# Performance work log

Measured on AMD Instinct MI355X. Metric: run time of the kernel, lower is better.

The kernel has to match this reference:

```python
import jax, jax.numpy as jnp
import numpy as np

D_MODEL = 2048
SEQ_LEN = 16   # R is built for context_window=16 in the original module
BATCH = 256


def make_rotary_matrix(m, d):
    # Faithful to get_rotary_matrix: theta = 10000 ** (-2*(i-1)/d)  (note the i-1 bug kept)
    pos = np.arange(m, dtype=np.float64)[:, None]            # [m,1]
    i = np.arange(d // 2, dtype=np.float64)[None, :]         # [1,d/2]
    theta = 10000.0 ** (-2.0 * (i - 1.0) / d)
    ang = pos * theta                                         # [m, d/2]
    cos, sin = np.cos(ang), np.sin(ang)
    R = np.zeros((m, d, d), dtype=np.float32)
    idx = np.arange(d // 2)
    R[:, 2 * idx, 2 * idx] = cos
    R[:, 2 * idx, 2 * idx + 1] = -sin
    R[:, 2 * idx + 1, 2 * idx] = sin
    R[:, 2 * idx + 1, 2 * idx + 1] = cos
    return jnp.asarray(R)


def setup_inputs() -> dict:
    key = jax.random.key(0)
    kx, kq, kk, kv = jax.random.split(key, 4)
    s = 1.0 / np.sqrt(D_MODEL)
    return {
        "x": jax.random.normal(kx, (BATCH, SEQ_LEN, D_MODEL), dtype=jnp.float32),
        "w_q": jax.random.normal(kq, (D_MODEL, D_MODEL), dtype=jnp.float32) * s,
        "w_k": jax.random.normal(kk, (D_MODEL, D_MODEL), dtype=jnp.float32) * s,
        "w_v": jax.random.normal(kv, (D_MODEL, D_MODEL), dtype=jnp.float32) * s,
    }


def reference(x, w_q, w_k, w_v):
    b, m, d = x.shape
    R = make_rotary_matrix(SEQ_LEN, d)[:m]                    # [m,d,d]
    # nn.Linear(bias=False): y = x @ W^T
    q = jnp.einsum("bmd,ed->bme", x, w_q)
    k = jnp.einsum("bmd,ed->bme", x, w_k)
    v = jnp.einsum("bmd,ed->bme", x, w_v)
    # dense per-position rotary rotation via bmm: (q.transpose(0,1) @ R[:m]).transpose(0,1)
    q_rot = jnp.einsum("bmd,mde->bme", q, R)
    k_rot = jnp.einsum("bmd,mde->bme", k, R)
    # scaled_dot_product_attention (dropout treated as eval-mode / disabled)
    scores = jnp.einsum("bme,bne->bmn", q_rot, k_rot) / jnp.sqrt(jnp.float32(d))
    attn = jax.nn.softmax(scores, axis=-1)
    return jnp.einsum("bmn,bne->bme", attn, v)
```

## Files before the change

### kernel.cpp

```cpp
#include <hip/hip_runtime.h>


#define D 2048
#define SEQLEN 16
#define NBATCH 256
#define NROWS (NBATCH * SEQLEN)
#define NX (NROWS * D)
#define NW (D * D)

#define BM 128
#define BN 192
#define BK 64
#define NKT (D / BK)
#define LDSPB ((BM + BN) * BK)

typedef __attribute__((ext_vector_type(8))) short bf16x8;
typedef __attribute__((ext_vector_type(4))) float f32x4;

__device__ __forceinline__ unsigned short f32_to_bf16(float f) {
  unsigned u = __float_as_uint(f);
  unsigned r = 0x7fffu + ((u >> 16) & 1u);
  return (unsigned short)((u + r) >> 16);
}
__device__ __forceinline__ float bf16lo_to_f32(unsigned u) { return __uint_as_float(u << 16); }
__device__ __forceinline__ float bf16hi_to_f32(unsigned u) { return __uint_as_float(u & 0xffff0000u); }

__device__ __forceinline__ bool detect_f32(const ushort* __restrict__ w) {
  int crazy = 0;
#pragma unroll
  for (int i = 0; i < 64; ++i) {
    float v = __uint_as_float((unsigned)w[i] << 16);
    if (!(__builtin_fabsf(v) < 256.0f)) ++crazy;
  }
  return crazy >= 3;
}

__device__ __forceinline__ void glds16(const void* g, void* l) {
  __builtin_amdgcn_global_load_lds(
      (const __attribute__((address_space(1))) void*)g,
      (__attribute__((address_space(3))) void*)l, 16, 0, 0);
}

__global__ __launch_bounds__(256) void convert_inputs(
    const void* __restrict__ x, const void* __restrict__ wq,
    const void* __restrict__ wk, const void* __restrict__ wv,
    ushort* __restrict__ xb, ushort* __restrict__ wqb,
    ushort* __restrict__ wkb, ushort* __restrict__ wvb) {
  if (!detect_f32((const ushort*)wq)) return;
  const float* srcs[4] = {(const float*)x, (const float*)wq, (const float*)wk, (const float*)wv};
  ushort* dsts[4] = {xb, wqb, wkb, wvb};
  const int ns[4] = {NX, NW, NW, NW};
  const int stride = gridDim.x * blockDim.x;
#pragma unroll
  for (int s = 0; s < 4; ++s) {
    const float* __restrict__ src = srcs[s];
    ushort* __restrict__ dst = dsts[s];
    const int n8 = ns[s] / 8;
    for (int i = blockIdx.x * blockDim.x + threadIdx.x; i < n8; i += stride) {
      float4 a = ((const float4*)src)[i * 2];
      float4 b = ((const float4*)src)[i * 2 + 1];
      uint4 o;
      o.x = (unsigned)f32_to_bf16(a.x) | ((unsigned)f32_to_bf16(a.y) << 16);
      o.y = (unsigned)f32_to_bf16(a.z) | ((unsigned)f32_to_bf16(a.w) << 16);
      o.z = (unsigned)f32_to_bf16(b.x) | ((unsigned)f32_to_bf16(b.y) << 16);
      o.w = (unsigned)f32_to_bf16(b.z) | ((unsigned)f32_to_bf16(b.w) << 16);
      ((uint4*)dst)[i] = o;
    }
  }
}

__global__ __launch_bounds__(256, 2) void qkv_rope_gemm(
    const void* __restrict__ Xr, const void* __restrict__ Wqr,
    const void* __restrict__ Wkr, const void* __restrict__ Wvr,
    const ushort* __restrict__ xb, const ushort* __restrict__ wqb,
    const ushort* __restrict__ wkb, const ushort* __restrict__ wvb,
    ushort* __restrict__ Ov, float* __restrict__ Sp) {
  __shared__ __align__(16) ushort lds[2][LDSPB];

  const bool f32in = detect_f32((const ushort*)Wqr);
  const ushort* __restrict__ X  = f32in ? xb  : (const ushort*)Xr;
  const ushort* __restrict__ Wq = f32in ? wqb : (const ushort*)Wqr;
  const ushort* __restrict__ Wk = f32in ? wkb : (const ushort*)Wkr;
  const ushort* __restrict__ Wv = f32in ? wvb : (const ushort*)Wvr;

  const int m0 = (blockIdx.x >> 5) * BM;
  const int eb = blockIdx.x & 31;
  const int e0 = eb * 64;

  const int t = threadIdx.x;
  const int wave = t >> 6, lane = t & 63;
  const int quad = lane >> 4, l16 = lane & 15;
  const int wr = wave >> 1, wc = wave & 1;

  const int srow = t >> 3;
  const int scol = ((t & 7) ^ (srow & 7)) * 8;
  const ushort* gA = X + (size_t)(m0 + srow) * D + scol;
  const ushort* gB[6];
#pragma unroll
  for (int c = 0; c < 6; ++c) {
    const ushort* Wz = (c < 2) ? Wq : (c < 4) ? Wk : Wv;
    gB[c] = Wz + (size_t)(e0 + (c & 1) * 32 + srow) * D + scol;
  }

  f32x4 acc[4][6] = {};

  auto STAGE = [&](int b, int kt) {
    const int kc = kt * BK;
#pragma unroll
    for (int c = 0; c < 4; ++c)
      glds16(gA + (size_t)c * 32 * D + kc, &lds[b][c * 2048 + t * 8]);
#pragma unroll
    for (int c = 0; c < 6; ++c)
      glds16(gB[c] + kc, &lds[b][BM * BK + c * 2048 + t * 8]);
  };

  STAGE(0, 0);
  STAGE(1, 1);

  const int swz = (l16 & 7) << 3;

  for (int kt = 0; kt < NKT; ++kt) {
    const int cur = kt & 1;

    if (kt < NKT - 1) asm volatile("s_waitcnt vmcnt(10)" ::: "memory");
    else              asm volatile("s_waitcnt vmcnt(0)"  ::: "memory");
    __builtin_amdgcn_s_barrier();
    __builtin_amdgcn_sched_barrier(0);

    const ushort* Ab = &lds[cur][0];
    const ushort* Bb = &lds[cur][BM * BK];

    bf16x8 af2[2][4], bfr2[2][6];
#pragma unroll
    for (int ks = 0; ks < 2; ++ks) {
      const int ko = (ks * 32 + quad * 8) ^ swz;
#pragma unroll
      for (int f = 0; f < 4; ++f)
        af2[ks][f] = *(const bf16x8*)(Ab + (wr * 64 + f * 16 + l16) * 64 + ko);
#pragma unroll
      for (int g = 0; g < 6; ++g)
        bfr2[ks][g] = *(const bf16x8*)(Bb + (wc * 96 + g * 16 + l16) * 64 + ko);
    }

    __builtin_amdgcn_s_setprio(1);
#pragma unroll
    for (int ks = 0; ks < 2; ++ks)
#pragma unroll
      for (int f = 0; f < 4; ++f)
#pragma unroll
        for (int g = 0; g < 6; ++g)
          acc[f][g] = __builtin_amdgcn_mfma_f32_16x16x32_bf16(
              af2[ks][f], bfr2[ks][g], acc[f][g], 0, 0, 0);
    __builtin_amdgcn_s_setprio(0);

    asm volatile("s_waitcnt lgkmcnt(0)" ::: "memory");
    __builtin_amdgcn_s_barrier();
    if (kt + 2 < NKT) STAGE(cur, kt + 2);
  }

  ushort* qk_lds = &lds[0][0];
#pragma unroll
  for (int g = 0; g < 6; ++g) {
    const int ncol = wc * 96 + g * 16;
    const int z = ncol >> 6;
    const int el = (ncol & 63) + l16;
    const int eg = e0 + el;
    if (z < 2) {
      const float theta = exp2f(-0.012976281620653759f * ((float)(eg >> 1) - 1.0f));
      float cs[4], sn[4];
#pragma unroll
      for (int r = 0; r < 4; ++r)
        __sincosf((float)(quad * 4 + r) * theta, &sn[r], &cs[r]);
#pragma unroll
      for (int f = 0; f < 4; ++f) {
#pragma unroll
        for (int r = 0; r < 4; ++r) {
          float v = acc[f][g][r];
          float p = __shfl_xor(v, 1);
          float o = (eg & 1) ? (v * cs[r] - p * sn[r])
                             : (v * cs[r] + p * sn[r]);
          const int row = wr * 64 + f * 16 + quad * 4 + r;
          const int colw = el ^ ((row & 7) << 3);
          qk_lds[z * 8192 + row * 64 + colw] = f32_to_bf16(o);
        }
      }
    } else {
#pragma unroll
      for (int f = 0; f < 4; ++f) {
        const size_t rbase = (size_t)(m0 + wr * 64 + f * 16 + quad * 4) * D;
#pragma unroll
        for (int r = 0; r < 4; ++r)
          Ov[rbase + (size_t)r * D + eg] = f32_to_bf16(acc[f][g][r]);
      }
    }
  }
  __syncthreads();

  const int gb0 = (m0 >> 4);
#pragma unroll
  for (int bb = 0; bb < 2; ++bb) {
    const int bi = wave * 2 + bb;
    const int row = bi * 16 + l16;
    f32x4 s = {0.f, 0.f, 0.f, 0.f};
#pragma unroll
    for (int ks = 0; ks < 2; ++ks) {
      const int ko = (ks * 32 + quad * 8) ^ swz;
      bf16x8 aq = *(const bf16x8*)(qk_lds + row * 64 + ko);
      bf16x8 bk = *(const bf16x8*)(qk_lds + 8192 + row * 64 + ko);
      s = __builtin_amdgcn_mfma_f32_16x16x32_bf16(aq, bk, s, 0, 0, 0);
    }
    float* sp = Sp + ((size_t)(eb * NBATCH + gb0 + bi) << 8);
#pragma unroll
    for (int r = 0; r < 4; ++r)
      sp[(quad * 4 + r) * 16 + l16] = s[r];
  }
}

__global__ __launch_bounds__(256) void rope_attention(
    const float* __restrict__ Sp, const ushort* __restrict__ V,
    const void* __restrict__ Wqr, void* __restrict__ OutRaw) {
  __shared__ float at[16][16];
  const bool f32out = detect_f32((const ushort*)Wqr);
  const int b = blockIdx.x;
  const int t = threadIdx.x;

  {
    const int m = t >> 4, n = t & 15;
    float s = 0.f;
#pragma unroll
    for (int ebi = 0; ebi < 32; ++ebi)
      s += Sp[((size_t)(ebi * NBATCH + b) << 8) + t];
    s *= 0.02209708691207961f;
    float mx = s;
#pragma unroll
    for (int off = 8; off; off >>= 1) mx = fmaxf(mx, __shfl_xor(mx, off, 16));
    float e = __expf(s - mx);
    float sum = e;
#pragma unroll
    for (int off = 8; off; off >>= 1) sum += __shfl_xor(sum, off, 16);
    at[m][n] = e / sum;
  }
  __syncthreads();

  const ushort* Vb = V + (size_t)b * (SEQLEN * D);
  const int e0 = t * 8;
  uint4 vr[16];
#pragma unroll
  for (int n = 0; n < 16; ++n)
    vr[n] = *(const uint4*)(Vb + n * D + e0);

  for (int m = 0; m < 16; ++m) {
    float av[8] = {0.f, 0.f, 0.f, 0.f, 0.f, 0.f, 0.f, 0.f};
#pragma unroll
    for (int n = 0; n < 16; ++n) {
      const float a = at[m][n];
      const uint4 u = vr[n];
      av[0] = fmaf(a, bf16lo_to_f32(u.x), av[0]);
      av[1] = fmaf(a, bf16hi_to_f32(u.x), av[1]);
      av[2] = fmaf(a, bf16lo_to_f32(u.y), av[2]);
      av[3] = fmaf(a, bf16hi_to_f32(u.y), av[3]);
      av[4] = fmaf(a, bf16lo_to_f32(u.z), av[4]);
      av[5] = fmaf(a, bf16hi_to_f32(u.z), av[5]);
      av[6] = fmaf(a, bf16lo_to_f32(u.w), av[6]);
      av[7] = fmaf(a, bf16hi_to_f32(u.w), av[7]);
    }
    if (f32out) {
      float* Ob = (float*)OutRaw + (size_t)b * (SEQLEN * D) + m * D + e0;
      float4 o0 = {av[0], av[1], av[2], av[3]};
      float4 o1 = {av[4], av[5], av[6], av[7]};
      ((float4*)Ob)[0] = o0;
      ((float4*)Ob)[1] = o1;
    } else {
      uint4 o;
      o.x = (unsigned)f32_to_bf16(av[0]) | ((unsigned)f32_to_bf16(av[1]) << 16);
      o.y = (unsigned)f32_to_bf16(av[2]) | ((unsigned)f32_to_bf16(av[3]) << 16);
      o.z = (unsigned)f32_to_bf16(av[4]) | ((unsigned)f32_to_bf16(av[5]) << 16);
      o.w = (unsigned)f32_to_bf16(av[6]) | ((unsigned)f32_to_bf16(av[7]) << 16);
      *(uint4*)((ushort*)OutRaw + (size_t)b * (SEQLEN * D) + m * D + e0) = o;
    }
  }
}

extern "C" void kernel_launch(void* const* d_in, const int* in_sizes, int n_in,
                              void* d_out, int out_size, void* d_ws, size_t ws_size,
                              hipStream_t stream) {
  const void* x  = d_in[0];
  const void* wq = d_in[1];
  const void* wk = d_in[2];
  const void* wv = d_in[3];
  ushort* ws = (ushort*)d_ws;
  ushort* xb  = ws;
  ushort* wqb = ws + NX;
  ushort* wkb = ws + NX + NW;
  ushort* wvb = ws + NX + 2 * (size_t)NW;
  ushort* v   = ws + NX + 3 * (size_t)NW;
  float*  Sp  = (float*)(ws + 2 * (size_t)NX + 3 * (size_t)NW);

  convert_inputs<<<1536, 256, 0, stream>>>(x, wq, wk, wv, xb, wqb, wkb, wvb);
  qkv_rope_gemm<<<dim3(1024), 256, 0, stream>>>(x, wq, wk, wv, xb, wqb, wkb, wvb, v, Sp);
  rope_attention<<<NBATCH, 256, 0, stream>>>(Sp, v, wq, (ushort*)d_out);
}
```

Measured before the change: 228.7 us.

## Fuse fp32-to-bf16 input conversion into the QKV GEMM main loop

Removes the separate conversion kernel and has the GEMM load fp32 tiles of X and the weights into registers, convert them to bf16 and write them into LDS inside a register-prefetched double-buffer pipeline. This avoids writing and re-reading the bf16 copies in global memory and saves one kernel launch. In exchange each GEMM block reads fp32 data, which doubles bytes per tile and repeats the conversion across blocks that share tiles. It also gives up the async global_load_lds path and uses more registers on the fp32 path. The bf16 path now uses a shallower single-stage prefetch.

```diff
diff --git a/kernel.cpp b/kernel.cpp
--- a/kernel.cpp
+++ b/kernel.cpp
@@ -41,47 +41,13 @@
       (__attribute__((address_space(3))) void*)l, 16, 0, 0);
 }
 
-__global__ __launch_bounds__(256) void convert_inputs(
-    const void* __restrict__ x, const void* __restrict__ wq,
-    const void* __restrict__ wk, const void* __restrict__ wv,
-    ushort* __restrict__ xb, ushort* __restrict__ wqb,
-    ushort* __restrict__ wkb, ushort* __restrict__ wvb) {
-  if (!detect_f32((const ushort*)wq)) return;
-  const float* srcs[4] = {(const float*)x, (const float*)wq, (const float*)wk, (const float*)wv};
-  ushort* dsts[4] = {xb, wqb, wkb, wvb};
-  const int ns[4] = {NX, NW, NW, NW};
-  const int stride = gridDim.x * blockDim.x;
-#pragma unroll
-  for (int s = 0; s < 4; ++s) {
-    const float* __restrict__ src = srcs[s];
-    ushort* __restrict__ dst = dsts[s];
-    const int n8 = ns[s] / 8;
-    for (int i = blockIdx.x * blockDim.x + threadIdx.x; i < n8; i += stride) {
-      float4 a = ((const float4*)src)[i * 2];
-      float4 b = ((const float4*)src)[i * 2 + 1];
-      uint4 o;
-      o.x = (unsigned)f32_to_bf16(a.x) | ((unsigned)f32_to_bf16(a.y) << 16);
-      o.y = (unsigned)f32_to_bf16(a.z) | ((unsigned)f32_to_bf16(a.w) << 16);
-      o.z = (unsigned)f32_to_bf16(b.x) | ((unsigned)f32_to_bf16(b.y) << 16);
-      o.w = (unsigned)f32_to_bf16(b.z) | ((unsigned)f32_to_bf16(b.w) << 16);
-      ((uint4*)dst)[i] = o;
-    }
-  }
-}
-
 __global__ __launch_bounds__(256, 2) void qkv_rope_gemm(
     const void* __restrict__ Xr, const void* __restrict__ Wqr,
     const void* __restrict__ Wkr, const void* __restrict__ Wvr,
-    const ushort* __restrict__ xb, const ushort* __restrict__ wqb,
-    const ushort* __restrict__ wkb, const ushort* __restrict__ wvb,
     ushort* __restrict__ Ov, float* __restrict__ Sp) {
   __shared__ __align__(16) ushort lds[2][LDSPB];
 
   const bool f32in = detect_f32((const ushort*)Wqr);
-  const ushort* __restrict__ X  = f32in ? xb  : (const ushort*)Xr;
-  const ushort* __restrict__ Wq = f32in ? wqb : (const ushort*)Wqr;
-  const ushort* __restrict__ Wk = f32in ? wkb : (const ushort*)Wkr;
-  const ushort* __restrict__ Wv = f32in ? wvb : (const ushort*)Wvr;
 
   const int m0 = (blockIdx.x >> 5) * BM;
   const int eb = blockIdx.x & 31;
@@ -94,68 +60,144 @@
 
   const int srow = t >> 3;
   const int scol = ((t & 7) ^ (srow & 7)) * 8;
-  const ushort* gA = X + (size_t)(m0 + srow) * D + scol;
-  const ushort* gB[6];
-#pragma unroll
-  for (int c = 0; c < 6; ++c) {
-    const ushort* Wz = (c < 2) ? Wq : (c < 4) ? Wk : Wv;
-    gB[c] = Wz + (size_t)(e0 + (c & 1) * 32 + srow) * D + scol;
-  }
+  const int swz = (l16 & 7) << 3;
 
   f32x4 acc[4][6] = {};
 
-  auto STAGE = [&](int b, int kt) {
-    const int kc = kt * BK;
-#pragma unroll
-    for (int c = 0; c < 4; ++c)
-      glds16(gA + (size_t)c * 32 * D + kc, &lds[b][c * 2048 + t * 8]);
-#pragma unroll
-    for (int c = 0; c < 6; ++c)
-      glds16(gB[c] + kc, &lds[b][BM * BK + c * 2048 + t * 8]);
-  };
-
-  STAGE(0, 0);
-  STAGE(1, 1);
-
-  const int swz = (l16 & 7) << 3;
-
-  for (int kt = 0; kt < NKT; ++kt) {
-    const int cur = kt & 1;
-
-    if (kt < NKT - 1) asm volatile("s_waitcnt vmcnt(10)" ::: "memory");
-    else              asm volatile("s_waitcnt vmcnt(0)"  ::: "memory");
-    __builtin_amdgcn_s_barrier();
-    __builtin_amdgcn_sched_barrier(0);
-
-    const ushort* Ab = &lds[cur][0];
-    const ushort* Bb = &lds[cur][BM * BK];
-
-    bf16x8 af2[2][4], bfr2[2][6];
-#pragma unroll
-    for (int ks = 0; ks < 2; ++ks) {
-      const int ko = (ks * 32 + quad * 8) ^ swz;
-#pragma unroll
-      for (int f = 0; f < 4; ++f)
-        af2[ks][f] = *(const bf16x8*)(Ab + (wr * 64 + f * 16 + l16) * 64 + ko);
-#pragma unroll
-      for (int g = 0; g < 6; ++g)
-        bfr2[ks][g] = *(const bf16x8*)(Bb + (wc * 96 + g * 16 + l16) * 64 + ko);
-    }
-
-    __builtin_amdgcn_s_setprio(1);
-#pragma unroll
-    for (int ks = 0; ks < 2; ++ks)
-#pragma unroll
-      for (int f = 0; f < 4; ++f)
-#pragma unroll
-        for (int g = 0; g < 6; ++g)
-          acc[f][g] = __builtin_amdgcn_mfma_f32_16x16x32_bf16(
-              af2[ks][f], bfr2[ks][g], acc[f][g], 0, 0, 0);
-    __builtin_amdgcn_s_setprio(0);
-
+  if (f32in) {
+    const float* __restrict__ Xf = (const float*)Xr;
+    const float* gAf = Xf + (size_t)(m0 + srow) * D + scol;
+    const float* gBf[6];
+#pragma unroll
+    for (int c = 0; c < 6; ++c) {
+      const float* Wz = (c < 2) ? (const float*)Wqr : (c < 4) ? (const float*)Wkr
+                                                              : (const float*)Wvr;
+      gBf[c] = Wz + (size_t)(e0 + (c & 1) * 32 + srow) * D + scol;
+    }
+
+    float4 R[10][2];
+    auto LD = [&](int kt) {
+      const int kc = kt * BK;
+#pragma unroll
+      for (int c = 0; c < 4; ++c) {
+        const float* p = gAf + (size_t)c * 32 * D + kc;
+        R[c][0] = *(const float4*)p;
+        R[c][1] = *(const float4*)(p + 4);
+      }
+#pragma unroll
+      for (int c = 0; c < 6; ++c) {
+        const float* p = gBf[c] + kc;
+        R[4 + c][0] = *(const float4*)p;
+        R[4 + c][1] = *(const float4*)(p + 4);
+      }
+    };
+    auto WR = [&](int b) {
+#pragma unroll
+      for (int c = 0; c < 10; ++c) {
+        uint4 o;
+        o.x = (unsigned)f32_to_bf16(R[c][0].x) | ((unsigned)f32_to_bf16(R[c][0].y) << 16);
+        o.y = (unsigned)f32_to_bf16(R[c][0].z) | ((unsigned)f32_to_bf16(R[c][0].w) << 16);
+        o.z = (unsigned)f32_to_bf16(R[c][1].x) | ((unsigned)f32_to_bf16(R[c][1].y) << 16);
+        o.w = (unsigned)f32_to_bf16(R[c][1].z) | ((unsigned)f32_to_bf16(R[c][1].w) << 16);
+        ushort* d = (c < 4) ? &lds[b][c * 2048 + t * 8]
+                            : &lds[b][BM * BK + (c - 4) * 2048 + t * 8];
+        *(uint4*)d = o;
+      }
+    };
+
+    LD(0);
+    asm volatile("s_waitcnt vmcnt(0)" ::: "memory");
+    WR(0);
+    LD(1);
     asm volatile("s_waitcnt lgkmcnt(0)" ::: "memory");
     __builtin_amdgcn_s_barrier();
-    if (kt + 2 < NKT) STAGE(cur, kt + 2);
+
+    for (int kt = 0; kt < NKT; ++kt) {
+      const int cur = kt & 1;
+      if (kt + 1 < NKT) {
+        asm volatile("s_waitcnt vmcnt(0)" ::: "memory");
+        WR(cur ^ 1);
+      }
+      if (kt + 2 < NKT) LD(kt + 2);
+
+      const ushort* Ab = &lds[cur][0];
+      const ushort* Bb = &lds[cur][BM * BK];
+#pragma unroll
+      for (int ks = 0; ks < 2; ++ks) {
+        const int ko = (ks * 32 + quad * 8) ^ swz;
+        bf16x8 af[4], bfr[6];
+#pragma unroll
+        for (int f = 0; f < 4; ++f)
+          af[f] = *(const bf16x8*)(Ab + (wr * 64 + f * 16 + l16) * 64 + ko);
+#pragma unroll
+        for (int g = 0; g < 6; ++g)
+          bfr[g] = *(const bf16x8*)(Bb + (wc * 96 + g * 16 + l16) * 64 + ko);
+        __builtin_amdgcn_s_setprio(1);
+#pragma unroll
+        for (int f = 0; f < 4; ++f)
+#pragma unroll
+          for (int g = 0; g < 6; ++g)
+            acc[f][g] = __builtin_amdgcn_mfma_f32_16x16x32_bf16(
+                af[f], bfr[g], acc[f][g], 0, 0, 0);
+        __builtin_amdgcn_s_setprio(0);
+      }
+      asm volatile("s_waitcnt lgkmcnt(0)" ::: "memory");
+      __builtin_amdgcn_s_barrier();
+    }
+  } else {
+    const ushort* __restrict__ X = (const ushort*)Xr;
+    const ushort* gA = X + (size_t)(m0 + srow) * D + scol;
+    const ushort* gB[6];
+#pragma unroll
+    for (int c = 0; c < 6; ++c) {
+      const ushort* Wz = (c < 2) ? (const ushort*)Wqr : (c < 4) ? (const ushort*)Wkr
+                                                                : (const ushort*)Wvr;
+      gB[c] = Wz + (size_t)(e0 + (c & 1) * 32 + srow) * D + scol;
+    }
+    auto STAGE = [&](int b, int kt) {
+      const int kc = kt * BK;
+#pragma unroll
+      for (int c = 0; c < 4; ++c)
+        glds16(gA + (size_t)c * 32 * D + kc, &lds[b][c * 2048 + t * 8]);
+#pragma unroll
+      for (int c = 0; c < 6; ++c)
+        glds16(gB[c] + kc, &lds[b][BM * BK + c * 2048 + t * 8]);
+    };
+
+    STAGE(0, 0);
+    asm volatile("s_waitcnt vmcnt(0)" ::: "memory");
+    __builtin_amdgcn_s_barrier();
+
+    for (int kt = 0; kt < NKT; ++kt) {
+      const int cur = kt & 1;
+      if (kt + 1 < NKT) STAGE(cur ^ 1, kt + 1);
+
+      const ushort* Ab = &lds[cur][0];
+      const ushort* Bb = &lds[cur][BM * BK];
+#pragma unroll
+      for (int ks = 0; ks < 2; ++ks) {
+        const int ko = (ks * 32 + quad * 8) ^ swz;
+        bf16x8 af[4], bfr[6];
+#pragma unroll
+        for (int f = 0; f < 4; ++f)
+          af[f] = *(const bf16x8*)(Ab + (wr * 64 + f * 16 + l16) * 64 + ko);
+#pragma unroll
+        for (int g = 0; g < 6; ++g)
+          bfr[g] = *(const bf16x8*)(Bb + (wc * 96 + g * 16 + l16) * 64 + ko);
+        __builtin_amdgcn_s_setprio(1);
+#pragma unroll
+        for (int f = 0; f < 4; ++f)
+#pragma unroll
+          for (int g = 0; g < 6; ++g)
+            acc[f][g] = __builtin_amdgcn_mfma_f32_16x16x32_bf16(
+                af[f], bfr[g], acc[f][g], 0, 0, 0);
+        __builtin_amdgcn_s_setprio(0);
+      }
+      if (kt + 1 < NKT)
+        asm volatile("s_waitcnt vmcnt(0)" ::: "memory");
+      asm volatile("s_waitcnt lgkmcnt(0)" ::: "memory");
+      __builtin_amdgcn_s_barrier();
+    }
   }
 
   ushort* qk_lds = &lds[0][0];
@@ -289,14 +331,9 @@
   const void* wk = d_in[2];
   const void* wv = d_in[3];
   ushort* ws = (ushort*)d_ws;
-  ushort* xb  = ws;
-  ushort* wqb = ws + NX;
-  ushort* wkb = ws + NX + NW;
-  ushort* wvb = ws + NX + 2 * (size_t)NW;
-  ushort* v   = ws + NX + 3 * (size_t)NW;
-  float*  Sp  = (float*)(ws + 2 * (size_t)NX + 3 * (size_t)NW);
-
-  convert_inputs<<<1536, 256, 0, stream>>>(x, wq, wk, wv, xb, wqb, wkb, wvb);
-  qkv_rope_gemm<<<dim3(1024), 256, 0, stream>>>(x, wq, wk, wv, xb, wqb, wkb, wvb, v, Sp);
+  ushort* v  = ws;
+  float*  Sp = (float*)(ws + (size_t)NX);
+
+  qkv_rope_gemm<<<dim3(1024), 256, 0, stream>>>(x, wq, wk, wv, v, Sp);
   rope_attention<<<NBATCH, 256, 0, stream>>>(Sp, v, wq, (ushort*)d_out);
 }
```

Result: slower. 292.3 us (+27.8%).
